# Optimization experiments

Hardware: AMD Instinct MI355X
Metric: run time of the kernel (lower is better)

## Reference

```python
import jax, jax.numpy as jnp
import numpy as np

N, IN, HID, OUT, C, H = 50000, 1488, 1024, 512, 32, 8
E = 800000

def setup_inputs() -> dict:
    key = jax.random.key(0)
    ks = jax.random.split(key, 16)
    s = lambda k, shape, fan: jax.random.normal(k, shape, jnp.float32) * (1.0 / np.sqrt(fan))
    return {
        "x": jax.random.normal(ks[0], (N, IN), jnp.float32),
        "edge_index": jax.random.randint(ks[1], (2, E), 0, N, jnp.int64),
        "ln_g": jnp.ones((IN,), jnp.float32),
        "ln_b": jnp.zeros((IN,), jnp.float32),
        "W1": s(ks[2], (IN, HID), IN), "b1": jnp.zeros((HID,), jnp.float32),
        "W2": s(ks[3], (HID, OUT), HID), "b2": jnp.zeros((OUT,), jnp.float32),
        "Wr": s(ks[4], (OUT, C * H), OUT), "br": jnp.zeros((C * H,), jnp.float32),
        "Wg": s(ks[5], (OUT, C * H), OUT),
        "att_src": s(ks[6], (H, C), C),
        "att_dst": s(ks[7], (H, C), C),
        "bg": jnp.zeros((C * H,), jnp.float32),
    }

def reference(x, edge_index, ln_g, ln_b, W1, b1, W2, b2, Wr, br, Wg, att_src, att_dst, bg):
    n = x.shape[0]
    # LayerNorm
    mu = jnp.mean(x, axis=-1, keepdims=True)
    var = jnp.mean(jnp.square(x - mu), axis=-1, keepdims=True)
    xn = (x - mu) * jax.lax.rsqrt(var + 1e-5) * ln_g + ln_b
    # init_proj MLP
    h = jax.nn.relu(xn @ W1 + b1) @ W2 + b2            # [N, OUT]
    res = h @ Wr + br                                   # [N, H*C]
    # GATConv (add_self_loops=True, dropout inactive in eval)
    loops = jnp.arange(n, dtype=edge_index.dtype)
    src = jnp.concatenate([edge_index[0], loops])
    dst = jnp.concatenate([edge_index[1], loops])
    g = (h @ Wg).reshape(n, H, C)                       # [N, H, C]
    a_src = jnp.sum(g * att_src, axis=-1)               # [N, H]
    a_dst = jnp.sum(g * att_dst, axis=-1)               # [N, H]
    e = jax.nn.leaky_relu(a_src[src] + a_dst[dst], 0.2) # [E', H]
    m = jax.ops.segment_max(e, dst, num_segments=n)     # per-dst softmax (stable)
    ex = jnp.exp(e - m[dst])
    denom = jax.ops.segment_sum(ex, dst, num_segments=n)
    alpha = ex / (denom[dst] + 1e-16)                   # [E', H]
    msg = alpha[:, :, None] * g[src]                    # [E', H, C]
    agg = jax.ops.segment_sum(msg, dst, num_segments=n) # [N, H, C]
    out = agg.reshape(n, H * C) + bg
    return jax.nn.elu(out) + res
```

## Files before the change

kernel.cpp:

```cpp
#include <hip/hip_runtime.h>
#include <hip/hip_bf16.h>
#include <cstdint>
#include <cstddef>

#define NND 50000
#define DIN 1488
#define DINP 1536
#define DHID 1024
#define DOUT 512
#define DHC 256
#define NE 800000
#define NHD 8

typedef __attribute__((ext_vector_type(8))) short short8;
typedef __attribute__((ext_vector_type(4))) short short4v;
typedef __attribute__((ext_vector_type(4))) float f32x4;
typedef __attribute__((ext_vector_type(4))) int int4v;
typedef unsigned short ushort_t;

__device__ __forceinline__ unsigned short f2bf(float f){
  union { float f; unsigned u; } v; v.f = f;
  unsigned r = v.u + 0x7fffu + ((v.u >> 16) & 1u);
  return (unsigned short)(r >> 16);
}
__device__ __forceinline__ float bf2f(unsigned short u){
  union { unsigned u; float f; } v; v.u = ((unsigned)u) << 16;
  return v.f;
}

__device__ __forceinline__ void async16(const void* g, void* l){
  __builtin_amdgcn_global_load_lds((__attribute__((address_space(1))) void*)g,
                                   (__attribute__((address_space(3))) void*)l, 16, 0, 0);
}

__device__ __forceinline__ void tc_tile(const float* __restrict__ W,
                                        ushort_t* __restrict__ WT,
                                        int K, int Nn, int Kp, int bx, int by){
  __shared__ float tile[32][33];
  const int tx = threadIdx.x & 31, ty = threadIdx.x >> 5;
  const int k0 = bx*32, n0 = by*32;
  for (int i = ty; i < 32; i += 8){
    int k = k0 + i, n = n0 + tx;
    tile[i][tx] = (k < K && n < Nn) ? W[(size_t)k*Nn + n] : 0.f;
  }
  __syncthreads();
  for (int i = ty; i < 32; i += 8){
    int n = n0 + i, k = k0 + tx;
    if (n < Nn && k < Kp) WT[(size_t)n*Kp + k] = f2bf(tile[tx][i]);
  }
}

#define F1_CNT  3125
#define F1_LN   (F1_CNT + 12500)
__global__ __launch_bounds__(256) void fused1(const float* __restrict__ x,
                                              const float* __restrict__ gw,
                                              const float* __restrict__ bw,
                                              ushort_t* __restrict__ xn,
                                              const int* __restrict__ ei,
                                              int* __restrict__ cnt,
                                              const float* W1, const float* Wr,
                                              const float* Wg, const float* W2,
                                              const float* b2, const float* br,
                                              ushort_t* W1T, ushort_t* WrgT,
                                              ushort_t* W2bf, float* b2rg){
  const int bid = blockIdx.x;
  if (bid < F1_CNT){
    int e = bid*256 + threadIdx.x;
    if (e < NE) atomicAdd(&cnt[ei[NE + e]], 1);
    return;
  }
  if (bid < F1_LN){
    const int wid = threadIdx.x >> 6, lane = threadIdx.x & 63;
    const int row = (bid - F1_CNT)*4 + wid;
    if (row >= NND) return;
    const float* xr = x + (size_t)row * DIN;
    f32x4 xa[3], xb[3];
    float s = 0.f, sq = 0.f;
    #pragma unroll
    for (int it = 0; it < 3; ++it){
      const int i = lane*8 + it*512;
      if (i < DIN){
        xa[it] = *(const f32x4*)(xr + i);
        xb[it] = *(const f32x4*)(xr + i + 4);
      } else {
        xa[it] = (f32x4){0.f,0.f,0.f,0.f};
        xb[it] = (f32x4){0.f,0.f,0.f,0.f};
      }
      s  += xa[it].x + xa[it].y + xa[it].z + xa[it].w
          + xb[it].x + xb[it].y + xb[it].z + xb[it].w;
      sq += xa[it].x*xa[it].x + xa[it].y*xa[it].y + xa[it].z*xa[it].z + xa[it].w*xa[it].w
          + xb[it].x*xb[it].x + xb[it].y*xb[it].y + xb[it].z*xb[it].z + xb[it].w*xb[it].w;
    }
    #pragma unroll
    for (int o = 32; o; o >>= 1){ s += __shfl_xor(s, o); sq += __shfl_xor(sq, o); }
    const float mu = s * (1.f/DIN);
    const float var = sq * (1.f/DIN) - mu*mu;
    const float rstd = rsqrtf(var + 1e-5f);
    ushort_t* xo = xn + (size_t)row * DINP;
    #pragma unroll
    for (int it = 0; it < 3; ++it){
      const int i = lane*8 + it*512;
      union { ushort_t u[8]; short8 v; } o;
      if (i < DIN){
        f32x4 ga = *(const f32x4*)(gw + i);
        f32x4 gb = *(const f32x4*)(gw + i + 4);
        f32x4 ba = *(const f32x4*)(bw + i);
        f32x4 bb = *(const f32x4*)(bw + i + 4);
        o.u[0] = f2bf((xa[it].x-mu)*rstd*ga.x + ba.x);
        o.u[1] = f2bf((xa[it].y-mu)*rstd*ga.y + ba.y);
        o.u[2] = f2bf((xa[it].z-mu)*rstd*ga.z + ba.z);
        o.u[3] = f2bf((xa[it].w-mu)*rstd*ga.w + ba.w);
        o.u[4] = f2bf((xb[it].x-mu)*rstd*gb.x + bb.x);
        o.u[5] = f2bf((xb[it].y-mu)*rstd*gb.y + bb.y);
        o.u[6] = f2bf((xb[it].z-mu)*rstd*gb.z + bb.z);
        o.u[7] = f2bf((xb[it].w-mu)*rstd*gb.w + bb.w);
      } else {
        o.u[0]=o.u[1]=o.u[2]=o.u[3]=o.u[4]=o.u[5]=o.u[6]=o.u[7]=0;
      }
      *(short8*)(xo + i) = o.v;
    }
    return;
  }
  {
    int b = bid - F1_LN;
    if (b < 1536){ tc_tile(W1, W1T, DIN, DHID, DINP, b % 48, b / 48); return; }
    b -= 1536;
    if (b < 128){ tc_tile(Wr, WrgT, DOUT, DHC, DOUT, b % 16, b / 16); return; }
    b -= 128;
    if (b < 128){ tc_tile(Wg, WrgT + 256*DOUT, DOUT, DHC, DOUT, b % 16, b / 16); return; }
    b -= 128;
    if (b < 256){
      const int idx = (b*256 + threadIdx.x)*8;
      f32x4 v0 = *(const f32x4*)(W2 + idx);
      f32x4 v1 = *(const f32x4*)(W2 + idx + 4);
      union { ushort_t u[8]; short8 s; } o;
      o.u[0]=f2bf(v0.x); o.u[1]=f2bf(v0.y); o.u[2]=f2bf(v0.z); o.u[3]=f2bf(v0.w);
      o.u[4]=f2bf(v1.x); o.u[5]=f2bf(v1.y); o.u[6]=f2bf(v1.z); o.u[7]=f2bf(v1.w);
      *(short8*)(W2bf + idx) = o.s;
      return;
    }
    b -= 256;
    {
      const int c = b*256 + threadIdx.x;
      float acc = 0.f;
      if (c < 256){
        for (int j = 0; j < DOUT; ++j) acc += b2[j]*Wr[(size_t)j*DHC + c];
        acc += br[c];
      } else {
        const int cc = c - 256;
        for (int j = 0; j < DOUT; ++j) acc += b2[j]*Wg[(size_t)j*DHC + cc];
      }
      b2rg[c] = acc;
      return;
    }
  }
}

__device__ __forceinline__ void g256p8_body(ushort_t (&lds)[2][2][2][64*128],
                                            const ushort_t* __restrict__ A,
                                            const ushort_t* __restrict__ BT,
                                            const float* __restrict__ bias,
                                            ushort_t* __restrict__ out0,
                                            int M, int Nn, int K,
                                            int bid, int nwg, bool act){
  const int t = threadIdx.x, wid = t >> 6, lane = t & 63;
  const int CB = Nn >> 8;
  const int q = nwg >> 3, r = nwg & 7;
  const int xcd = bid & 7, slot = bid >> 3;
  const int lg = (xcd < r ? xcd*(q+1) : r*(q+1) + (xcd - r)*q) + slot;
  const int brow = (lg / CB) * 256, bcol = (lg % CB) * 256;

  const int l8  = t >> 3;
  const int cb  = (t & 7) << 4;
  const unsigned scb = (unsigned)(cb ^ ((l8 & 7) << 4));
  unsigned rowA[2][2], rowB[2][2];
  #pragma unroll
  for (int hf = 0; hf < 2; ++hf)
    #pragma unroll
    for (int rd = 0; rd < 2; ++rd){
      int ra = brow + hf*128 + rd*64 + l8; ra = ra < M ? ra : M-1;
      int rb = bcol + hf*128 + rd*64 + l8; rb = rb < Nn ? rb : Nn-1;
      rowA[hf][rd] = (unsigned)ra * (unsigned)(K*2);
      rowB[hf][rd] = (unsigned)rb * (unsigned)(K*2);
    }
  const int w8 = wid * 8;

#define STG_A(buf, hf, kt) do {                                               \
    const unsigned _ob = (unsigned)(kt)*128u + scb;                           \
    async16((const char*)A + rowA[hf][0] + _ob, &lds[buf][0][hf][(w8)*64]);   \
    async16((const char*)A + rowA[hf][1] + _ob, &lds[buf][0][hf][(64+w8)*64]);\
  } while(0)
#define STG_B(buf, hf, kt) do {                                               \
    const unsigned _ob = (unsigned)(kt)*128u + scb;                           \
    async16((const char*)BT + rowB[hf][0] + _ob, &lds[buf][1][hf][(w8)*64]);  \
    async16((const char*)BT + rowB[hf][1] + _ob, &lds[buf][1][hf][(64+w8)*64]);\
  } while(0)

  f32x4 acc[8][4];
  #pragma unroll
  for (int i=0;i<8;i++)
    #pragma unroll
    for (int j=0;j<4;j++) acc[i][j] = (f32x4){0.f,0.f,0.f,0.f};

  const int wrow = (wid >> 2), wcol = (wid & 3);
  const int fr = lane & 15;
  const int kb0 = (lane >> 4) << 4;
  const int sx  = (fr & 7) << 4;
  const int ko0 = ((kb0      ) ^ sx) >> 1;
  const int ko1 = ((kb0 | 64 ) ^ sx) >> 1;
  const int bhalf = wcol >> 1, brl = (wcol & 1)*64;

#define RD_A(buf, m) do {                                          \
    const int _ra = ((m)*16 + fr)*64;                              \
    af[m][0] = *(const short8*)&lds[buf][0][wrow][_ra + ko0];      \
    af[m][1] = *(const short8*)&lds[buf][0][wrow][_ra + ko1];      \
  } while(0)
#define RD_B(buf, n) do {                                          \
    const int _rb = (brl + (n)*16 + fr)*64;                        \
    bf[n][0] = *(const short8*)&lds[buf][1][bhalf][_rb + ko0];     \
    bf[n][1] = *(const short8*)&lds[buf][1][bhalf][_rb + ko1];     \
  } while(0)
#define SYNC_PH() do {                                             \
    __builtin_amdgcn_s_barrier();                                  \
    asm volatile("s_waitcnt lgkmcnt(0)" ::: "memory");             \
    __builtin_amdgcn_sched_barrier(0);                             \
  } while(0)
#define MFMA_Q(M0, N0) do {                                        \
    __builtin_amdgcn_s_setprio(1);                                 \
    _Pragma("unroll")                                              \
    for (int _m=(M0); _m<(M0)+4; ++_m)                             \
      _Pragma("unroll")                                            \
      for (int _n=(N0); _n<(N0)+2; ++_n){                          \
        acc[_m][_n] = __builtin_amdgcn_mfma_f32_16x16x32_bf16(af[_m][0], bf[_n][0], acc[_m][_n], 0, 0, 0); \
        acc[_m][_n] = __builtin_amdgcn_mfma_f32_16x16x32_bf16(af[_m][1], bf[_n][1], acc[_m][_n], 0, 0, 0); \
      }                                                            \
    __builtin_amdgcn_s_setprio(0);                                 \
  } while(0)

  const int nk = K >> 6;
  STG_A(0,0,0); STG_A(0,1,0); STG_B(0,0,0); STG_B(0,1,0);
  STG_A(1,0,1); STG_A(1,1,1);
  asm volatile("s_waitcnt vmcnt(4)" ::: "memory");
  __builtin_amdgcn_s_barrier();

  for (int kt = 0; kt < nk; ++kt){
    const int buf = kt & 1, obuf = buf ^ 1;
    short8 af[8][2], bf[4][2];
    RD_A(buf,0); RD_A(buf,1); RD_A(buf,2); RD_A(buf,3);
    RD_B(buf,0); RD_B(buf,1);
    if (kt + 1 < nk) STG_B(obuf, 0, kt + 1);
    SYNC_PH();
    MFMA_Q(0, 0);
    RD_A(buf,4); RD_A(buf,5); RD_A(buf,6); RD_A(buf,7);
    if (kt + 1 < nk) STG_B(obuf, 1, kt + 1);
    SYNC_PH();
    MFMA_Q(4, 0);
    RD_B(buf,2); RD_B(buf,3);
    if (kt + 2 < nk) STG_A(buf, 0, kt + 2);
    SYNC_PH();
    MFMA_Q(0, 2);
    if (kt + 2 < nk){
      STG_A(buf, 1, kt + 2);
      asm volatile("s_waitcnt vmcnt(4)" ::: "memory");
    } else {
      asm volatile("s_waitcnt vmcnt(0)" ::: "memory");
    }
    __builtin_amdgcn_s_barrier();
    MFMA_Q(4, 2);
  }

  float bv[4];
  #pragma unroll
  for (int n=0;n<4;n++){
    const int col = bcol + wcol*64 + n*16 + (lane & 15);
    bv[n] = bias ? bias[col] : 0.f;
  }
  ushort_t* sB = (ushort_t*)&lds[0][0][0][0];
  __syncthreads();
  #pragma unroll
  for (int m=0;m<8;m++){
    const int row = wrow*128 + m*16 + (lane >> 4)*4;
    #pragma unroll
    for (int n=0;n<4;n++){
      const int col = wcol*64 + n*16 + (lane & 15);
      #pragma unroll
      for (int j=0;j<4;j++){
        float v = acc[m][n][j] + bv[n];
        if (act) v = v > 0.f ? v : 0.f;
        sB[(row+j)*256 + col] = f2bf(v);
      }
    }
  }
  __syncthreads();
  const int srow = t >> 5, scol8 = (t & 31) * 8;
  #pragma unroll
  for (int rr = 0; rr < 16; ++rr){
    const int rloc = rr*16 + srow;
    const int grow = brow + rloc;
    if (grow < M)
      *(short8*)(out0 + (size_t)grow*Nn + bcol + scol8) = *(const short8*)&sB[rloc*256 + scol8];
  }
}

__global__ __launch_bounds__(512, 1) void mega_gemm(const ushort_t* __restrict__ xn,
                                                    const ushort_t* __restrict__ W1T,
                                                    const float* __restrict__ b1,
                                                    ushort_t* __restrict__ h1,
                                                    const ushort_t* __restrict__ WrgT,
                                                    const ushort_t* __restrict__ W2bf,
                                                    ushort_t* __restrict__ WcT,
                                                    const int* __restrict__ cnt,
                                                    int* __restrict__ offs,
                                                    int* __restrict__ cur){
  __shared__ __align__(16) ushort_t lds[2][2][2][64*128];
  const int t = threadIdx.x;

  if (blockIdx.x == 0){
    int* sbuf = (int*)&lds[0][0][0][0];
    const int chunk = (NND + 255) >> 8;
    int s = 0;
    if (t < 256){
      const int s0 = t*chunk;
      const int s1 = (s0 + chunk < NND) ? s0 + chunk : NND;
      for (int i = s0; i < s1; i += 4){
        int4v v = *(const int4v*)(cnt + i);
        s += v.x + v.y + v.z + v.w + 4;
      }
    }
    sbuf[t] = s; __syncthreads();
    for (int o = 1; o < 256; o <<= 1){
      int xv = (t >= o && t < 256) ? sbuf[t-o] : 0;
      __syncthreads();
      if (t < 256) sbuf[t] += xv;
      __syncthreads();
    }
    if (t < 256){
      int run = sbuf[t] - s;
      const int s0 = t*chunk;
      const int s1 = (s0 + chunk < NND) ? s0 + chunk : NND;
      for (int i = s0; i < s1; i += 4){
        int4v v = *(const int4v*)(cnt + i);
        int4v cu;
        cu.x = run; run += v.x + 1;
        cu.y = run; run += v.y + 1;
        cu.z = run; run += v.z + 1;
        cu.w = run; run += v.w + 1;
        *(int4v*)(cur + i)  = cu;
        *(int4v*)(offs + i) = cu;
      }
      if (t == 255) offs[NND] = run;
    }
    return;
  }
  if (blockIdx.x < 9){
    g256p8_body(lds, WrgT, W2bf, nullptr, WcT, 512, 1024, 512,
                (int)blockIdx.x - 1, 8, false);
    return;
  }
  g256p8_body(lds, xn, W1T, b1, h1, NND, DHID, DINP,
              (int)blockIdx.x - 9, (int)gridDim.x - 9, true);
}

#define G3_NWG 392
__global__ __launch_bounds__(512, 1) void gemm3p8(const ushort_t* __restrict__ A,
                                                  const ushort_t* __restrict__ BT,
                                                  const float* __restrict__ bias,
                                                  float* __restrict__ res,
                                                  ushort_t* __restrict__ gm,
                                                  const int* __restrict__ ei,
                                                  int* __restrict__ cur,
                                                  int* __restrict__ eidx,
                                                  const float* __restrict__ att_s,
                                                  const float* __restrict__ att_d,
                                                  float* __restrict__ asrc,
                                                  float* __restrict__ adst){
  __shared__ __align__(16) ushort_t lds[2][2][2][64*128];
  const int t = threadIdx.x, wid = t >> 6, lane = t & 63;

  if (blockIdx.x >= G3_NWG){
    int i = (blockIdx.x - G3_NWG)*512 + t;
    if (i < NND){
      int p = atomicAdd(&cur[i], 1); eidx[p] = i;
    } else if (i < NND + NE){
      int e = i - NND;
      int src = ei[e], dst = ei[NE + e];
      int p = atomicAdd(&cur[dst], 1);
      eidx[p] = src;
    }
    return;
  }

  const int M = NND, Nn = 512, K = DHID;
  const int bid = blockIdx.x, nwg = G3_NWG;
  const int CB = 2;
  const int q = nwg >> 3, r = nwg & 7;
  const int xcd = bid & 7, slot = bid >> 3;
  const int lg = (xcd < r ? xcd*(q+1) : r*(q+1) + (xcd - r)*q) + slot;
  const int brow = (lg / CB) * 256, bcol = (lg % CB) * 256;

  const int l8  = t >> 3;
  const int cb  = (t & 7) << 4;
  const unsigned scb = (unsigned)(cb ^ ((l8 & 7) << 4));
  unsigned rowA[2][2], rowB[2][2];
  #pragma unroll
  for (int hf = 0; hf < 2; ++hf)
    #pragma unroll
    for (int rd = 0; rd < 2; ++rd){
      int ra = brow + hf*128 + rd*64 + l8; ra = ra < M ? ra : M-1;
      int rb = bcol + hf*128 + rd*64 + l8; rb = rb < Nn ? rb : Nn-1;
      rowA[hf][rd] = (unsigned)ra * (unsigned)(K*2);
      rowB[hf][rd] = (unsigned)rb * (unsigned)(K*2);
    }
  const int w8 = wid * 8;

  f32x4 acc[8][4];
  #pragma unroll
  for (int i=0;i<8;i++)
    #pragma unroll
    for (int j=0;j<4;j++) acc[i][j] = (f32x4){0.f,0.f,0.f,0.f};

  const int wrow = (wid >> 2), wcol = (wid & 3);
  const int fr = lane & 15;
  const int kb0 = (lane >> 4) << 4;
  const int sx  = (fr & 7) << 4;
  const int ko0 = ((kb0      ) ^ sx) >> 1;
  const int ko1 = ((kb0 | 64 ) ^ sx) >> 1;
  const int bhalf = wcol >> 1, brl = (wcol & 1)*64;

  const int nk = K >> 6;
  STG_A(0,0,0); STG_A(0,1,0); STG_B(0,0,0); STG_B(0,1,0);
  STG_A(1,0,1); STG_A(1,1,1);
  asm volatile("s_waitcnt vmcnt(4)" ::: "memory");
  __builtin_amdgcn_s_barrier();

  for (int kt = 0; kt < nk; ++kt){
    const int buf = kt & 1, obuf = buf ^ 1;
    short8 af[8][2], bf[4][2];
    RD_A(buf,0); RD_A(buf,1); RD_A(buf,2); RD_A(buf,3);
    RD_B(buf,0); RD_B(buf,1);
    if (kt + 1 < nk) STG_B(obuf, 0, kt + 1);
    SYNC_PH();
    MFMA_Q(0, 0);
    RD_A(buf,4); RD_A(buf,5); RD_A(buf,6); RD_A(buf,7);
    if (kt + 1 < nk) STG_B(obuf, 1, kt + 1);
    SYNC_PH();
    MFMA_Q(4, 0);
    RD_B(buf,2); RD_B(buf,3);
    if (kt + 2 < nk) STG_A(buf, 0, kt + 2);
    SYNC_PH();
    MFMA_Q(0, 2);
    if (kt + 2 < nk){
      STG_A(buf, 1, kt + 2);
      asm volatile("s_waitcnt vmcnt(4)" ::: "memory");
    } else {
      asm volatile("s_waitcnt vmcnt(0)" ::: "memory");
    }
    __builtin_amdgcn_s_barrier();
    MFMA_Q(4, 2);
  }
#undef STG_A
#undef STG_B
#undef RD_A
#undef RD_B
#undef SYNC_PH
#undef MFMA_Q

  float bv[4];
  #pragma unroll
  for (int n=0;n<4;n++){
    const int col = bcol + wcol*64 + n*16 + (lane & 15);
    bv[n] = bias[col];
  }
  if (bcol == 0){
    float* sF = (float*)&lds[0][0][0][0];
    #pragma unroll
    for (int p = 0; p < 2; ++p){
      __syncthreads();
      if (wrow == p){
        #pragma unroll
        for (int m=0;m<8;m++){
          const int row = m*16 + (lane >> 4)*4;
          #pragma unroll
          for (int n=0;n<4;n++){
            const int col = wcol*64 + n*16 + (lane & 15);
            #pragma unroll
            for (int j=0;j<4;j++)
              sF[(row+j)*256 + col] = acc[m][n][j] + bv[n];
          }
        }
      }
      __syncthreads();
      const int srow = t >> 6, scol4 = (t & 63) * 4;
      #pragma unroll
      for (int rr = 0; rr < 16; ++rr){
        const int rloc = rr*8 + srow;
        const int grow = brow + p*128 + rloc;
        if (grow < M)
          *(f32x4*)(res + (size_t)grow*256 + scol4) = *(const f32x4*)&sF[rloc*256 + scol4];
      }
    }
  } else {
    ushort_t* sB = (ushort_t*)&lds[0][0][0][0];
    __syncthreads();
    #pragma unroll
    for (int m=0;m<8;m++){
      const int row = wrow*128 + m*16 + (lane >> 4)*4;
      #pragma unroll
      for (int n=0;n<4;n++){
        const int col = wcol*64 + n*16 + (lane & 15);
        #pragma unroll
        for (int j=0;j<4;j++)
          sB[(row+j)*256 + col] = f2bf(acc[m][n][j] + bv[n]);
      }
    }
    __syncthreads();
    const int srow = t >> 5, scol8 = (t & 31) * 8;
    #pragma unroll
    for (int rr = 0; rr < 16; ++rr){
      const int rloc = rr*16 + srow;
      const int grow = brow + rloc;
      if (grow < M)
        *(short8*)(gm + (size_t)grow*256 + scol8) = *(const short8*)&sB[rloc*256 + scol8];
    }
    const int h = t & 7;
    const int hc0 = h * 32;
    #pragma unroll
    for (int k = 0; k < 4; ++k){
      const int rloc = (t >> 3) + k*64;
      const int grow = brow + rloc;
      if (grow < M){
        float a = 0.f, d = 0.f;
        #pragma unroll
        for (int c0 = 0; c0 < 32; c0 += 8){
          short8 gv = *(const short8*)&sB[rloc*256 + hc0 + c0];
          #pragma unroll
          for (int j = 0; j < 8; ++j){
            float g = bf2f((ushort_t)gv[j]);
            a += g*att_s[hc0 + c0 + j];
            d += g*att_d[hc0 + c0 + j];
          }
        }
        asrc[grow*NHD + h] = a;
        adst[grow*NHD + h] = d;
      }
    }
  }
}

__global__ __launch_bounds__(256) void gat_agg(const int* __restrict__ offs,
                                               const int* __restrict__ eidx,
                                               const float* __restrict__ asrc,
                                               const float* __restrict__ adst,
                                               const ushort_t* __restrict__ gm,
                                               const float* __restrict__ res,
                                               const float* __restrict__ bg,
                                               float* __restrict__ out){
  const int wid = threadIdx.x >> 6, lane = threadIdx.x & 63;
  const int node = blockIdx.x*4 + wid;
  if (node >= NND) return;
  const int h = lane >> 3, jj = lane & 7;
  const int e0 = offs[node], deg = offs[node+1] - e0;
  const float adv = adst[node*NHD + h];

  float mx = -1e30f;
  for (int j = jj; j < deg; j += 8){
    int s = eidx[e0 + j];
    float e = asrc[s*NHD + h] + adv; e = e > 0.f ? e : 0.2f*e;
    mx = fmaxf(mx, e);
  }
  mx = fmaxf(mx, __shfl_xor(mx, 1));
  mx = fmaxf(mx, __shfl_xor(mx, 2));
  mx = fmaxf(mx, __shfl_xor(mx, 4));

  const int c4 = lane*4;
  float sm = 0.f;
  f32x4 acc = {0.f,0.f,0.f,0.f};
  for (int j0 = 0; j0 < deg; j0 += 8){
    const int cnt = (deg - j0) < 8 ? (deg - j0) : 8;
    int s = 0; float w = 0.f;
    if (jj < cnt){
      s = eidx[e0 + j0 + jj];
      float e = asrc[s*NHD + h] + adv; e = e > 0.f ? e : 0.2f*e;
      w = __expf(e - mx);
      sm += w;
    }
    #pragma unroll
    for (int u = 0; u < 8; ++u){
      if (u < cnt){
        const int   su = __builtin_amdgcn_readlane(s, u);
        const float wu = __shfl(w, (h << 3) | u);
        short4v gv = *(const short4v*)(gm + (size_t)su*DHC + c4);
        acc.x += wu*bf2f((ushort_t)gv.x);
        acc.y += wu*bf2f((ushort_t)gv.y);
        acc.z += wu*bf2f((ushort_t)gv.z);
        acc.w += wu*bf2f((ushort_t)gv.w);
      }
    }
  }
  sm += __shfl_xor(sm, 1); sm += __shfl_xor(sm, 2); sm += __shfl_xor(sm, 4);
  const float inv = 1.f/(sm + 1e-16f);

  f32x4 bgv = *(const f32x4*)(bg + c4);
  f32x4 rv  = *(const f32x4*)(res + (size_t)node*DHC + c4);
  f32x4 o;
  #pragma unroll
  for (int q = 0; q < 4; ++q){
    float v = acc[q]*inv + bgv[q];
    v = v > 0.f ? v : expm1f(v);
    o[q] = v + rv[q];
  }
  *(f32x4*)(out + (size_t)node*DHC + c4) = o;
}

extern "C" void kernel_launch(void* const* d_in, const int* in_sizes, int n_in,
                              void* d_out, int out_size, void* d_ws, size_t ws_size,
                              hipStream_t stream){
  (void)in_sizes; (void)n_in; (void)out_size; (void)ws_size;
  const float* x     = (const float*)d_in[0];
  const int*   ei    = (const int*)d_in[1];
  const float* ln_g  = (const float*)d_in[2];
  const float* ln_b  = (const float*)d_in[3];
  const float* W1    = (const float*)d_in[4];
  const float* b1    = (const float*)d_in[5];
  const float* W2    = (const float*)d_in[6];
  const float* b2    = (const float*)d_in[7];
  const float* Wr    = (const float*)d_in[8];
  const float* br    = (const float*)d_in[9];
  const float* Wg    = (const float*)d_in[10];
  const float* att_s = (const float*)d_in[11];
  const float* att_d = (const float*)d_in[12];
  const float* bg    = (const float*)d_in[13];
  float* out = (float*)d_out;

  char* p = (char*)d_ws;
  ushort_t* xn   = (ushort_t*)(p);
  ushort_t* h1   = (ushort_t*)(p + 153600000);
  float*    asrc = (float*)(p + 256000000);
  float*    adst = (float*)(p + 257600000);
  int*      cnt  = (int*)(p + 259200000);
  int*      offs = (int*)(p + 259400064);
  int*      cur  = (int*)(p + 259600128);
  int*      eidx = (int*)(p + 259800192);
  ushort_t* W1T  = (ushort_t*)d_out;
  ushort_t* WrgT = (ushort_t*)((char*)d_out + 3145728);
  ushort_t* W2bf = (ushort_t*)((char*)d_out + 3670016);
  ushort_t* WcT  = (ushort_t*)((char*)d_out + 4718592);
  float*    b2rg = (float*)((char*)d_out + 5767168);
  float*    res  = (float*)(p + 0);
  ushort_t* gm   = (ushort_t*)(p + 51200000);

  hipMemsetAsync(cnt, 0, NND*sizeof(int), stream);

  fused1<<<F1_LN + 2050, 256, 0, stream>>>(
      x, ln_g, ln_b, xn, ei, cnt,
      W1, Wr, Wg, W2, b2, br, W1T, WrgT, W2bf, b2rg);

  mega_gemm<<<793, 512, 0, stream>>>(xn, W1T, b1, h1, WrgT, W2bf, WcT,
                                     cnt, offs, cur);

  gemm3p8<<<G3_NWG + (NND + NE + 511)/512, 512, 0, stream>>>(
      h1, WcT, b2rg, res, gm,
      ei, cur, eidx, att_s, att_d, asrc, adst);

  gat_agg<<<(NND + 3)/4, 256, 0, stream>>>(offs, eidx, asrc, adst, gm, res, bg, out);
}
```

Measured before the change: 481.8 us.

## Vectorize degree counting, reorder mega_gemm blocks, prefetch next edge batch in aggregation

The edge-degree counting loads four destination indices per thread with one int4 load and issues four atomics, which cuts the counting block count by four. In mega_gemm the large W1 GEMM tiles now take the low block indices, and the scan block and the small Wc GEMM blocks move to the end of the grid. This changes dispatch order so the big tiles start first. The GAT aggregation loop now loads and exponentiates the next group of eight edges before doing the gathers for the current group, overlapping index and score latency with the feature gathers. The gemm3p8 macros are redefined locally after being undefined, which is a cleanup.

```diff
diff --git a/kernel.cpp b/kernel.cpp
--- a/kernel.cpp
+++ b/kernel.cpp
@@ -50,7 +50,7 @@
   }
 }
 
-#define F1_CNT  3125
+#define F1_CNT  782
 #define F1_LN   (F1_CNT + 12500)
 __global__ __launch_bounds__(256) void fused1(const float* __restrict__ x,
                                               const float* __restrict__ gw,
@@ -65,8 +65,12 @@
                                               ushort_t* W2bf, float* b2rg){
   const int bid = blockIdx.x;
   if (bid < F1_CNT){
-    int e = bid*256 + threadIdx.x;
-    if (e < NE) atomicAdd(&cnt[ei[NE + e]], 1);
+    int i4 = bid*256 + threadIdx.x;
+    if (i4 < NE/4){
+      int4v v = *(const int4v*)(ei + NE + i4*4);
+      atomicAdd(&cnt[v.x], 1); atomicAdd(&cnt[v.y], 1);
+      atomicAdd(&cnt[v.z], 1); atomicAdd(&cnt[v.w], 1);
+    }
     return;
   }
   if (bid < F1_LN){
@@ -268,6 +272,12 @@
     __builtin_amdgcn_s_barrier();
     MFMA_Q(4, 2);
   }
+#undef STG_A
+#undef STG_B
+#undef RD_A
+#undef RD_B
+#undef SYNC_PH
+#undef MFMA_Q
 
   float bv[4];
   #pragma unroll
@@ -302,6 +312,7 @@
   }
 }
 
+#define G1_NWG 784
 __global__ __launch_bounds__(512, 1) void mega_gemm(const ushort_t* __restrict__ xn,
                                                     const ushort_t* __restrict__ W1T,
                                                     const float* __restrict__ b1,
@@ -315,7 +326,7 @@
   __shared__ __align__(16) ushort_t lds[2][2][2][64*128];
   const int t = threadIdx.x;
 
-  if (blockIdx.x == 0){
+  if (blockIdx.x == G1_NWG){
     int* sbuf = (int*)&lds[0][0][0][0];
     const int chunk = (NND + 255) >> 8;
     int s = 0;
@@ -352,13 +363,13 @@
     }
     return;
   }
-  if (blockIdx.x < 9){
+  if (blockIdx.x > G1_NWG){
     g256p8_body(lds, WrgT, W2bf, nullptr, WcT, 512, 1024, 512,
-                (int)blockIdx.x - 1, 8, false);
+                (int)blockIdx.x - (G1_NWG + 1), 8, false);
     return;
   }
   g256p8_body(lds, xn, W1T, b1, h1, NND, DHID, DINP,
-              (int)blockIdx.x - 9, (int)gridDim.x - 9, true);
+              (int)blockIdx.x, G1_NWG, true);
 }
 
 #define G3_NWG 392
@@ -413,6 +424,17 @@
     }
   const int w8 = wid * 8;
 
+#define STG_A(buf, hf, kt) do {                                               \
+    const unsigned _ob = (unsigned)(kt)*128u + scb;                           \
+    async16((const char*)A + rowA[hf][0] + _ob, &lds[buf][0][hf][(w8)*64]);   \
+    async16((const char*)A + rowA[hf][1] + _ob, &lds[buf][0][hf][(64+w8)*64]);\
+  } while(0)
+#define STG_B(buf, hf, kt) do {                                               \
+    const unsigned _ob = (unsigned)(kt)*128u + scb;                           \
+    async16((const char*)BT + rowB[hf][0] + _ob, &lds[buf][1][hf][(w8)*64]);  \
+    async16((const char*)BT + rowB[hf][1] + _ob, &lds[buf][1][hf][(64+w8)*64]);\
+  } while(0)
+
   f32x4 acc[8][4];
   #pragma unroll
   for (int i=0;i<8;i++)
@@ -426,6 +448,33 @@
   const int ko0 = ((kb0      ) ^ sx) >> 1;
   const int ko1 = ((kb0 | 64 ) ^ sx) >> 1;
   const int bhalf = wcol >> 1, brl = (wcol & 1)*64;
+
+#define RD_A(buf, m) do {                                          \
+    const int _ra = ((m)*16 + fr)*64;                              \
+    af[m][0] = *(const short8*)&lds[buf][0][wrow][_ra + ko0];      \
+    af[m][1] = *(const short8*)&lds[buf][0][wrow][_ra + ko1];      \
+  } while(0)
+#define RD_B(buf, n) do {                                          \
+    const int _rb = (brl + (n)*16 + fr)*64;                        \
+    bf[n][0] = *(const short8*)&lds[buf][1][bhalf][_rb + ko0];     \
+    bf[n][1] = *(const short8*)&lds[buf][1][bhalf][_rb + ko1];     \
+  } while(0)
+#define SYNC_PH() do {                                             \
+    __builtin_amdgcn_s_barrier();                                  \
+    asm volatile("s_waitcnt lgkmcnt(0)" ::: "memory");             \
+    __builtin_amdgcn_sched_barrier(0);                             \
+  } while(0)
+#define MFMA_Q(M0, N0) do {                                        \
+    __builtin_amdgcn_s_setprio(1);                                 \
+    _Pragma("unroll")                                              \
+    for (int _m=(M0); _m<(M0)+4; ++_m)                             \
+      _Pragma("unroll")                                            \
+      for (int _n=(N0); _n<(N0)+2; ++_n){                          \
+        acc[_m][_n] = __builtin_amdgcn_mfma_f32_16x16x32_bf16(af[_m][0], bf[_n][0], acc[_m][_n], 0, 0, 0); \
+        acc[_m][_n] = __builtin_amdgcn_mfma_f32_16x16x32_bf16(af[_m][1], bf[_n][1], acc[_m][_n], 0, 0, 0); \
+      }                                                            \
+    __builtin_amdgcn_s_setprio(0);                                 \
+  } while(0)
 
   const int nk = K >> 6;
   STG_A(0,0,0); STG_A(0,1,0); STG_B(0,0,0); STG_B(0,1,0);
@@ -575,14 +624,26 @@
   const int c4 = lane*4;
   float sm = 0.f;
   f32x4 acc = {0.f,0.f,0.f,0.f};
-  for (int j0 = 0; j0 < deg; j0 += 8){
-    const int cnt = (deg - j0) < 8 ? (deg - j0) : 8;
-    int s = 0; float w = 0.f;
-    if (jj < cnt){
-      s = eidx[e0 + j0 + jj];
+
+  int s = 0; float w = 0.f;
+  {
+    const int cnt0 = deg < 8 ? deg : 8;
+    if (jj < cnt0){
+      s = eidx[e0 + jj];
       float e = asrc[s*NHD + h] + adv; e = e > 0.f ? e : 0.2f*e;
       w = __expf(e - mx);
       sm += w;
+    }
+  }
+  for (int j0 = 0; j0 < deg; j0 += 8){
+    const int cnt = (deg - j0) < 8 ? (deg - j0) : 8;
+    int ns = 0; float nw = 0.f;
+    const int ncnt = (deg - j0 - 8) < 8 ? (deg - j0 - 8) : 8;
+    if (jj < ncnt){
+      ns = eidx[e0 + j0 + 8 + jj];
+      float e = asrc[ns*NHD + h] + adv; e = e > 0.f ? e : 0.2f*e;
+      nw = __expf(e - mx);
+      sm += nw;
     }
     #pragma unroll
     for (int u = 0; u < 8; ++u){
@@ -596,6 +657,7 @@
         acc.w += wu*bf2f((ushort_t)gv.w);
       }
     }
+    s = ns; w = nw;
   }
   sm += __shfl_xor(sm, 1); sm += __shfl_xor(sm, 2); sm += __shfl_xor(sm, 4);
   const float inv = 1.f/(sm + 1e-16f);
@@ -655,8 +717,8 @@
       x, ln_g, ln_b, xn, ei, cnt,
       W1, Wr, Wg, W2, b2, br, W1T, WrgT, W2bf, b2rg);
 
-  mega_gemm<<<793, 512, 0, stream>>>(xn, W1T, b1, h1, WrgT, W2bf, WcT,
-                                     cnt, offs, cur);
+  mega_gemm<<<G1_NWG + 9, 512, 0, stream>>>(xn, W1T, b1, h1, WrgT, W2bf, WcT,
+                                            cnt, offs, cur);
 
   gemm3p8<<<G3_NWG + (NND + NE + 511)/512, 512, 0, stream>>>(
       h1, WcT, b2rg, res, gm,
```

New measurement: 496.2 us. 1.03x slower.
